# Kernel optimization log

Hardware: AMD Instinct MI355X
Metric: run time of the kernel (lower is better)

Reference implementation:

```python
import jax, jax.numpy as jnp
import numpy as np

WS = 32          # window_size
STRIDE = 16
OUTPUT = 224
GRADE_N = 6

def _dct_mat(size):
    i = np.arange(size)[:, None]
    j = np.arange(size)[None, :]
    scale = np.where(i == 0, np.sqrt(1.0 / size), np.sqrt(2.0 / size))
    return (scale * np.cos((j + 0.5) * np.pi * i / size)).astype(np.float32)

def _gen_filter(start, end, size):
    i = np.arange(size)[:, None]
    j = np.arange(size)[None, :]
    s = i + j
    return np.where((s > end) | (s < start), 0.0, 1.0).astype(np.float32)

# constant (non-learnable) buffers, derived from init hyperparams
_D = jnp.asarray(_dct_mat(WS))                       # [32,32]
_LEVEL_FILT = jnp.asarray(_gen_filter(0, WS * 2, WS))  # level_fliter=[0] -> band (0, 64)
_grade_filts = np.stack([_gen_filter(WS * 2.0 / GRADE_N * i, WS * 2.0 / GRADE_N * (i + 1), WS)
                         for i in range(GRADE_N)])    # [G,32,32]
_ft_num = _grade_filts.sum(axis=(1, 2))               # per-filter normalizer
_weights = (2.0 ** np.arange(GRADE_N)).astype(np.float32)  # w=1, *=2 each pass
_GRADE_FILT_SCALED = jnp.asarray(_grade_filts * (_weights / _ft_num)[:, None, None])  # [G,32,32]

def _unfold(x):
    # x: [B,C,H,W] -> patches [B,L,C,ws,ws], L row-major over (oh, ow), matching torch Unfold
    B, C, H, W = x.shape
    nH = (H - WS) // STRIDE + 1
    nW = (W - WS) // STRIDE + 1
    r = jnp.arange(nH) * STRIDE
    c = jnp.arange(nW) * STRIDE
    rows = r[:, None, None, None] + jnp.arange(WS)[None, None, :, None]  # [nH,1,ws,1]
    cols = c[None, :, None, None] + jnp.arange(WS)[None, None, None, :]  # [1,nW,1,ws]
    p = x[:, :, rows, cols]                       # [B,C,nH,nW,ws,ws]
    p = jnp.transpose(p, (0, 2, 3, 1, 4, 5))      # [B,nH,nW,C,ws,ws]
    return p.reshape(B, nH * nW, C, WS, WS)

def setup_inputs() -> dict:
    key = jax.random.key(0)
    x = jax.random.normal(key, (16, 3, 512, 512), dtype=jnp.float32)
    return {"x": x}

def reference(x):
    B, C, H, W = x.shape
    patches = _unfold(x)                          # [B,L,C,32,32]
    x_dct = _D @ patches @ _D.T                   # batched 32x32 DCT

    # level branch (level_N=1): filter is all-pass band (0,64) but applied faithfully
    level_y = _D.T @ (x_dct * _LEVEL_FILT) @ _D   # [B,L,C,32,32]

    # grading: sum_g w_g/ft_g * sum_{c,i,j} filt_g * log(|dct|+1)
    lx = jnp.log(jnp.abs(x_dct) + 1.0)
    grade = jnp.einsum('blcij,gij->bl', lx, _GRADE_FILT_SCALED)  # [B,L]

    idx = jnp.argsort(grade, axis=-1)             # ascending
    b = jnp.arange(B)
    minmin_i  = idx[:, 0]
    minmin_i1 = idx[:, 1]    # B > 1 branch
    maxmax_i  = idx[:, -1]
    maxmax_i1 = idx[:, -2]   # B > 1 branch

    # gather single patch per image; fold0 with one block == reshape to [B,C,32,32]
    x_minmin  = level_y[b, minmin_i]
    x_maxmax  = level_y[b, maxmax_i]
    x_minmin1 = level_y[b, minmin_i1]
    x_maxmax1 = level_y[b, maxmax_i1]
    return (x_minmin, x_maxmax, x_minmin1, x_maxmax1)
```

## Files before the change

kernel.cpp:

```cpp
#include <hip/hip_runtime.h>
#include <cstdint>

constexpr double kPI  = 3.14159265358979323846264338327950288;
constexpr double kLN2 = 0.69314718055994530941723212145818;
constexpr double cos_poly(double x) {
    double x2 = x * x, term = 1.0, sum = 1.0;
    for (int n = 1; n <= 13; ++n) { term *= -x2 / double((2 * n - 1) * (2 * n)); sum += term; }
    return sum;
}
constexpr double cos_idx(int a) {
    a &= 127;
    if (a <= 32)  return  cos_poly(a * kPI / 64.0);
    if (a <= 64)  return -cos_poly((64 - a) * kPI / 64.0);
    if (a <= 96)  return -cos_poly((a - 64) * kPI / 64.0);
    return cos_poly((128 - a) * kPI / 64.0);
}
constexpr double csqrt(double v) {
    double x = 1.0;
    for (int i = 0; i < 60; ++i) x = 0.5 * (x + v / x);
    return x;
}
constexpr float Dij(int i, int j) {
    double sc = (i == 0) ? csqrt(1.0 / 32.0) : 0.25;
    int a = ((2 * j + 1) * i) & 127;
    return (float)(sc * cos_idx(a));
}
struct OddT { float d[256]; };
constexpr OddT make_odd() { OddT t{}; for (int m = 0; m < 16; ++m) for (int k = 0; k < 16; ++k) t.d[m*16+k] = Dij(2*m+1, k); return t; }
struct E8T { float d[64]; };
constexpr E8T make_e2() { E8T t{}; for (int m = 0; m < 8; ++m) for (int k = 0; k < 8; ++k) t.d[m*8+k] = Dij(4*m+2, k); return t; }
struct E4T { float d[16]; };
constexpr E4T make_ee() { E4T t{}; for (int m = 0; m < 4; ++m) for (int k = 0; k < 4; ++k) t.d[m*4+k] = Dij(8*m,   k); return t; }
constexpr E4T make_eo() { E4T t{}; for (int m = 0; m < 4; ++m) for (int k = 0; k < 4; ++k) t.d[m*4+k] = Dij(8*m+4, k); return t; }
struct FTab { float f[64]; };
constexpr FTab make_F() {
    FTab t{};
    const int lo[6] = {0, 11, 22, 32, 43, 54};
    const int hi[6] = {10, 21, 32, 42, 53, 62};
    const int n [6] = {66, 187, 306, 286, 165, 45};
    for (int s = 0; s < 64; ++s) {
        double acc = 0.0, w = 1.0;
        for (int g = 0; g < 6; ++g) { if (s >= lo[g] && s <= hi[g]) acc += w / double(n[g]); w *= 2.0; }
        t.f[s] = (float)(acc * kLN2);
    }
    return t;
}
__device__ constexpr OddT cOdd = make_odd();
__device__ constexpr E8T  cE2  = make_e2();
__device__ constexpr E4T  cEE  = make_ee();
__device__ constexpr E4T  cEO  = make_eo();
__device__ constexpr FTab cF   = make_F();

#define NP  15376
#define NPC 46128
#define LPB 961
#define SST 34

template <typename EMIT>
__device__ __forceinline__ void dct32(float* __restrict__ v, EMIT&& emit) {
    #pragma unroll
    for (int k = 0; k < 16; ++k) { float a = v[k], b = v[31-k]; v[k] = a + b; v[31-k] = a - b; }
    #pragma unroll
    for (int k = 0; k < 8; ++k)  { float a = v[k], b = v[15-k]; v[k] = a + b; v[15-k] = a - b; }
    #pragma unroll
    for (int k = 0; k < 4; ++k)  { float a = v[k], b = v[7-k];  v[k] = a + b; v[7-k]  = a - b; }
    #pragma unroll
    for (int m = 0; m < 16; m += 2) {
        float a = 0.f, b = 0.f;
        #pragma unroll
        for (int k = 0; k < 16; ++k) {
            a = fmaf(cOdd.d[m*16+k],     v[31-k], a);
            b = fmaf(cOdd.d[(m+1)*16+k], v[31-k], b);
        }
        emit(2*m+1, a); emit(2*m+3, b);
    }
    #pragma unroll
    for (int m = 0; m < 8; m += 2) {
        float a = 0.f, b = 0.f;
        #pragma unroll
        for (int k = 0; k < 8; ++k) {
            a = fmaf(cE2.d[m*8+k],     v[15-k], a);
            b = fmaf(cE2.d[(m+1)*8+k], v[15-k], b);
        }
        emit(4*m+2, a); emit(4*m+6, b);
    }
    {
        float a0=0.f,a1=0.f,a2=0.f,a3=0.f,b0=0.f,b1=0.f,b2=0.f,b3=0.f;
        #pragma unroll
        for (int k = 0; k < 4; ++k) {
            a0 = fmaf(cEE.d[0*4+k], v[k],   a0);
            a1 = fmaf(cEE.d[1*4+k], v[k],   a1);
            a2 = fmaf(cEE.d[2*4+k], v[k],   a2);
            a3 = fmaf(cEE.d[3*4+k], v[k],   a3);
            b0 = fmaf(cEO.d[0*4+k], v[7-k], b0);
            b1 = fmaf(cEO.d[1*4+k], v[7-k], b1);
            b2 = fmaf(cEO.d[2*4+k], v[7-k], b2);
            b3 = fmaf(cEO.d[3*4+k], v[7-k], b3);
        }
        emit(0, a0); emit(8, a1); emit(16, a2); emit(24, a3);
        emit(4, b0); emit(12, b1); emit(20, b2); emit(28, b3);
    }
}

__global__ __launch_bounds__(64, 4) void k_grade(const float* __restrict__ x,
                                                 float* __restrict__ partial) {
    __shared__ __align__(16) float sS[2][32 * SST];
    __shared__ float sF[64];
    const int tid = threadIdx.x, g = tid >> 5, lane = tid & 31;
    sF[tid] = cF.f[tid];

    const int tc   = blockIdx.x * 2 + g;
    const int task = tc / 3, c = tc - task * 3;
    const int b  = task / LPB;
    const int l  = task - b * LPB;
    const int ph = l / 31, pw = l - ph * 31;
    const float4* row = (const float4*)(x + (size_t)(b * 3 + c) * 262144
                                          + (ph * 16 + lane) * 512 + pw * 16);
    float* S = sS[g];

    float p[32];
    #pragma unroll
    for (int q = 0; q < 8; ++q) {
        float4 f = row[q];
        p[4*q] = f.x; p[4*q+1] = f.y; p[4*q+2] = f.z; p[4*q+3] = f.w;
    }
    dct32(p, [&](int j, float acc) { S[j * SST + lane] = acc; });
    __syncthreads();

    float u[32];
    #pragma unroll
    for (int h = 0; h < 16; ++h) {
        float2 uu = *(const float2*)&S[lane * SST + 2 * h];
        u[2*h] = uu.x; u[2*h+1] = uu.y;
    }
    float gsum = 0.0f;
    dct32(u, [&](int i, float z) {
        gsum = fmaf(__log2f(fabsf(z) + 1.0f), sF[i + lane], gsum);
    });
    #pragma unroll
    for (int off = 16; off > 0; off >>= 1) gsum += __shfl_down(gsum, off, 32);
    if (lane == 0) partial[tc] = gsum;
}

__global__ __launch_bounds__(256) void k_selgather(const float* __restrict__ partial,
                                                   const float* __restrict__ x,
                                                   float* __restrict__ out) {
    __shared__ unsigned long long smx1[256], smx2[256], smn1[256], smn2[256];
    __shared__ int ssel[4];
    const int b = blockIdx.x, tid = threadIdx.x;
    unsigned long long mx1 = 0, mx2 = 0, mn1 = ~0ULL, mn2 = ~0ULL;
    for (int l = tid; l < LPB; l += 256) {
        const float* pp = partial + (size_t)(b * LPB + l) * 3;
        float gr = pp[0] + pp[1] + pp[2];
        unsigned int bits = __float_as_uint(gr);
        unsigned long long k = ((unsigned long long)bits << 32) | (unsigned int)l;
        if (k > mx1) { mx2 = mx1; mx1 = k; } else if (k > mx2) { mx2 = k; }
        if (k < mn1) { mn2 = mn1; mn1 = k; } else if (k < mn2) { mn2 = k; }
    }
    smx1[tid] = mx1; smx2[tid] = mx2; smn1[tid] = mn1; smn2[tid] = mn2;
    for (int off = 128; off > 0; off >>= 1) {
        __syncthreads();
        if (tid < off) {
            unsigned long long a1 = smx1[tid], a2 = smx2[tid], b1 = smx1[tid + off], b2 = smx2[tid + off];
            unsigned long long lo = a1 < b1 ? a1 : b1, hi = a1 < b1 ? b1 : a1;
            unsigned long long c2 = a2 > b2 ? a2 : b2;
            smx1[tid] = hi; smx2[tid] = lo > c2 ? lo : c2;
            a1 = smn1[tid]; a2 = smn2[tid]; b1 = smn1[tid + off]; b2 = smn2[tid + off];
            lo = a1 < b1 ? a1 : b1; hi = a1 < b1 ? b1 : a1;
            c2 = a2 < b2 ? a2 : b2;
            smn1[tid] = lo; smn2[tid] = hi < c2 ? hi : c2;
        }
    }
    __syncthreads();
    if (tid == 0) {
        ssel[0] = (int)(smn1[0] & 0xffffffffu);
        ssel[1] = (int)(smx1[0] & 0xffffffffu);
        ssel[2] = (int)(smn2[0] & 0xffffffffu);
        ssel[3] = (int)(smx2[0] & 0xffffffffu);
    }
    __syncthreads();

    #pragma unroll
    for (int it = 0; it < 12; ++it) {
        const int q  = it * 256 + tid;
        const int o  = q / 768;
        const int r2 = q - o * 768;
        const int c  = r2 >> 8;
        const int p  = r2 & 255;
        const int i  = p >> 3, j4 = p & 7;
        const int l  = ssel[o];
        const int r0 = (l / 31) * 16, c0 = (l - (l / 31) * 31) * 16;
        const float4 v = *(const float4*)(x + ((size_t)(b * 3 + c) * 512 + r0 + i) * 512 + c0 + 4 * j4);
        *(float4*)(out + (size_t)o * 49152 + b * 3072 + c * 1024 + i * 32 + 4 * j4) = v;
    }
}

extern "C" void kernel_launch(void* const* d_in, const int* in_sizes, int n_in,
                              void* d_out, int out_size, void* d_ws, size_t ws_size,
                              hipStream_t stream) {
    const float* x = (const float*)d_in[0];
    float* out     = (float*)d_out;
    float* partial = (float*)d_ws;
    k_grade    <<<NPC / 2, 64, 0, stream>>>(x, partial);
    k_selgather<<<16,     256, 0, stream>>>(partial, x, out);
}
```

Baseline: 111.7 us.

## Compute patch DCTs with fp16 MFMA instead of scalar butterfly FMAs

Replaces the per-lane scalar butterfly DCT with two stages of 16x16x32 fp16 MFMA matrix multiplies, one full 64-lane wave per patch-channel. A small init kernel prepares fp16 DCT-matrix fragments in workspace, and the grade weights are indexed to match the MFMA output layout. This cuts the FMA-bound arithmetic, but casting inputs and intermediates to fp16 lowers precision and could change the argsort selection on near-ties. It also adds an extra kernel launch.

After: 106.2 us. 1.05x faster.

```diff
diff --git a/kernel.cpp b/kernel.cpp
--- a/kernel.cpp
+++ b/kernel.cpp
@@ -1,5 +1,8 @@
 #include <hip/hip_runtime.h>
 #include <cstdint>
+
+typedef _Float16 f16x8 __attribute__((ext_vector_type(8)));
+typedef float    f32x4 __attribute__((ext_vector_type(4)));
 
 constexpr double kPI  = 3.14159265358979323846264338327950288;
 constexpr double kLN2 = 0.69314718055994530941723212145818;
@@ -20,18 +23,17 @@
     for (int i = 0; i < 60; ++i) x = 0.5 * (x + v / x);
     return x;
 }
-constexpr float Dij(int i, int j) {
-    double sc = (i == 0) ? csqrt(1.0 / 32.0) : 0.25;
-    int a = ((2 * j + 1) * i) & 127;
-    return (float)(sc * cos_idx(a));
-}
-struct OddT { float d[256]; };
-constexpr OddT make_odd() { OddT t{}; for (int m = 0; m < 16; ++m) for (int k = 0; k < 16; ++k) t.d[m*16+k] = Dij(2*m+1, k); return t; }
-struct E8T { float d[64]; };
-constexpr E8T make_e2() { E8T t{}; for (int m = 0; m < 8; ++m) for (int k = 0; k < 8; ++k) t.d[m*8+k] = Dij(4*m+2, k); return t; }
-struct E4T { float d[16]; };
-constexpr E4T make_ee() { E4T t{}; for (int m = 0; m < 4; ++m) for (int k = 0; k < 4; ++k) t.d[m*4+k] = Dij(8*m,   k); return t; }
-constexpr E4T make_eo() { E4T t{}; for (int m = 0; m < 4; ++m) for (int k = 0; k < 4; ++k) t.d[m*4+k] = Dij(8*m+4, k); return t; }
+struct DTab { float d[1024]; };
+constexpr DTab make_D() {
+    DTab t{};
+    const double s0 = csqrt(1.0 / 32.0);
+    for (int i = 0; i < 32; ++i) {
+        double sc = (i == 0) ? s0 : 0.25;
+        for (int j = 0; j < 32; ++j)
+            t.d[i * 32 + j] = (float)(sc * cos_idx(((2 * j + 1) * i) & 127));
+    }
+    return t;
+}
 struct FTab { float f[64]; };
 constexpr FTab make_F() {
     FTab t{};
@@ -45,100 +47,102 @@
     }
     return t;
 }
-__device__ constexpr OddT cOdd = make_odd();
-__device__ constexpr E8T  cE2  = make_e2();
-__device__ constexpr E4T  cEE  = make_ee();
-__device__ constexpr E4T  cEO  = make_eo();
-__device__ constexpr FTab cF   = make_F();
+__device__ constexpr DTab cD = make_D();
+__device__ constexpr FTab cF = make_F();
 
 #define NP  15376
 #define NPC 46128
 #define LPB 961
-#define SST 34
-
-template <typename EMIT>
-__device__ __forceinline__ void dct32(float* __restrict__ v, EMIT&& emit) {
-    #pragma unroll
-    for (int k = 0; k < 16; ++k) { float a = v[k], b = v[31-k]; v[k] = a + b; v[31-k] = a - b; }
-    #pragma unroll
-    for (int k = 0; k < 8; ++k)  { float a = v[k], b = v[15-k]; v[k] = a + b; v[15-k] = a - b; }
-    #pragma unroll
-    for (int k = 0; k < 4; ++k)  { float a = v[k], b = v[7-k];  v[k] = a + b; v[7-k]  = a - b; }
-    #pragma unroll
-    for (int m = 0; m < 16; m += 2) {
-        float a = 0.f, b = 0.f;
+#define TP  36
+
+__global__ __launch_bounds__(128) void k_init(_Float16* __restrict__ dfrag) {
+    const int t = threadIdx.x;
+    const int tile = t >> 6, lane = t & 63;
+    const int m  = 16 * tile + (lane & 15);
+    const int k0 = ((lane >> 4) & 3) * 8;
+    #pragma unroll
+    for (int j = 0; j < 8; ++j)
+        dfrag[t * 8 + j] = (_Float16)cD.d[m * 32 + k0 + j];
+}
+
+__global__ __launch_bounds__(128, 4) void k_grade(const float* __restrict__ x,
+                                                  const _Float16* __restrict__ dfrag,
+                                                  float* __restrict__ partial) {
+    __shared__ __align__(16) float sT[2][32 * TP];
+    __shared__ float sF[64];
+    const int tid  = threadIdx.x;
+    const int wv   = tid >> 6, lane = tid & 63;
+    const int quad = lane >> 4, n = lane & 15;
+    if (tid < 64) sF[tid] = cF.f[tid];
+
+    const int tc   = blockIdx.x * 2 + wv;
+    const int task = tc / 3, c = tc - task * 3;
+    const int b  = task / LPB, l = task - b * LPB;
+    const int ph = l / 31, pw = l - ph * 31;
+
+    const f16x8* DF = (const f16x8*)dfrag;
+    const f16x8 d0 = DF[lane], d1 = DF[64 + lane];
+
+    const float* pp = x + (size_t)(b * 3 + c) * 262144
+                        + (size_t)(ph * 16 + quad * 8) * 512 + pw * 16 + n;
+    f16x8 p0, p1;
+    #pragma unroll
+    for (int j = 0; j < 8; ++j) {
+        p0[j] = (_Float16)pp[j * 512];
+        p1[j] = (_Float16)pp[j * 512 + 16];
+    }
+
+    const f32x4 z4 = {0.f, 0.f, 0.f, 0.f};
+    f32x4 t00 = __builtin_amdgcn_mfma_f32_16x16x32_f16(d0, p0, z4, 0, 0, 0);
+    f32x4 t01 = __builtin_amdgcn_mfma_f32_16x16x32_f16(d0, p1, z4, 0, 0, 0);
+    f32x4 t10 = __builtin_amdgcn_mfma_f32_16x16x32_f16(d1, p0, z4, 0, 0, 0);
+    f32x4 t11 = __builtin_amdgcn_mfma_f32_16x16x32_f16(d1, p1, z4, 0, 0, 0);
+
+    float* S = sT[wv];
+    #pragma unroll
+    for (int r = 0; r < 4; ++r) {
+        S[(quad * 4 + r) * TP + n]           = t00[r];
+        S[(quad * 4 + r) * TP + 16 + n]      = t01[r];
+        S[(16 + quad * 4 + r) * TP + n]      = t10[r];
+        S[(16 + quad * 4 + r) * TP + 16 + n] = t11[r];
+    }
+    __syncthreads();
+
+    f16x8 a0, a1;
+    {
+        const float* rp = &S[n * TP + quad * 8];
+        const float4 x0 = *(const float4*)(rp);
+        const float4 x1 = *(const float4*)(rp + 4);
+        const float4 x2 = *(const float4*)(rp + 16 * TP);
+        const float4 x3 = *(const float4*)(rp + 16 * TP + 4);
+        a0[0]=(_Float16)x0.x; a0[1]=(_Float16)x0.y; a0[2]=(_Float16)x0.z; a0[3]=(_Float16)x0.w;
+        a0[4]=(_Float16)x1.x; a0[5]=(_Float16)x1.y; a0[6]=(_Float16)x1.z; a0[7]=(_Float16)x1.w;
+        a1[0]=(_Float16)x2.x; a1[1]=(_Float16)x2.y; a1[2]=(_Float16)x2.z; a1[3]=(_Float16)x2.w;
+        a1[4]=(_Float16)x3.x; a1[5]=(_Float16)x3.y; a1[6]=(_Float16)x3.z; a1[7]=(_Float16)x3.w;
+    }
+
+    f32x4 q00 = __builtin_amdgcn_mfma_f32_16x16x32_f16(a0, d0, z4, 0, 0, 0);
+    f32x4 q01 = __builtin_amdgcn_mfma_f32_16x16x32_f16(a0, d1, z4, 0, 0, 0);
+    f32x4 q10 = __builtin_amdgcn_mfma_f32_16x16x32_f16(a1, d0, z4, 0, 0, 0);
+    f32x4 q11 = __builtin_amdgcn_mfma_f32_16x16x32_f16(a1, d1, z4, 0, 0, 0);
+
+    const int sb = quad * 4 + n;
+    float W[12];
+    #pragma unroll
+    for (int t2 = 0; t2 < 3; ++t2)
         #pragma unroll
-        for (int k = 0; k < 16; ++k) {
-            a = fmaf(cOdd.d[m*16+k],     v[31-k], a);
-            b = fmaf(cOdd.d[(m+1)*16+k], v[31-k], b);
-        }
-        emit(2*m+1, a); emit(2*m+3, b);
-    }
-    #pragma unroll
-    for (int m = 0; m < 8; m += 2) {
-        float a = 0.f, b = 0.f;
-        #pragma unroll
-        for (int k = 0; k < 8; ++k) {
-            a = fmaf(cE2.d[m*8+k],     v[15-k], a);
-            b = fmaf(cE2.d[(m+1)*8+k], v[15-k], b);
-        }
-        emit(4*m+2, a); emit(4*m+6, b);
-    }
-    {
-        float a0=0.f,a1=0.f,a2=0.f,a3=0.f,b0=0.f,b1=0.f,b2=0.f,b3=0.f;
-        #pragma unroll
-        for (int k = 0; k < 4; ++k) {
-            a0 = fmaf(cEE.d[0*4+k], v[k],   a0);
-            a1 = fmaf(cEE.d[1*4+k], v[k],   a1);
-            a2 = fmaf(cEE.d[2*4+k], v[k],   a2);
-            a3 = fmaf(cEE.d[3*4+k], v[k],   a3);
-            b0 = fmaf(cEO.d[0*4+k], v[7-k], b0);
-            b1 = fmaf(cEO.d[1*4+k], v[7-k], b1);
-            b2 = fmaf(cEO.d[2*4+k], v[7-k], b2);
-            b3 = fmaf(cEO.d[3*4+k], v[7-k], b3);
-        }
-        emit(0, a0); emit(8, a1); emit(16, a2); emit(24, a3);
-        emit(4, b0); emit(12, b1); emit(20, b2); emit(28, b3);
-    }
-}
-
-__global__ __launch_bounds__(64, 4) void k_grade(const float* __restrict__ x,
-                                                 float* __restrict__ partial) {
-    __shared__ __align__(16) float sS[2][32 * SST];
-    __shared__ float sF[64];
-    const int tid = threadIdx.x, g = tid >> 5, lane = tid & 31;
-    sF[tid] = cF.f[tid];
-
-    const int tc   = blockIdx.x * 2 + g;
-    const int task = tc / 3, c = tc - task * 3;
-    const int b  = task / LPB;
-    const int l  = task - b * LPB;
-    const int ph = l / 31, pw = l - ph * 31;
-    const float4* row = (const float4*)(x + (size_t)(b * 3 + c) * 262144
-                                          + (ph * 16 + lane) * 512 + pw * 16);
-    float* S = sS[g];
-
-    float p[32];
-    #pragma unroll
-    for (int q = 0; q < 8; ++q) {
-        float4 f = row[q];
-        p[4*q] = f.x; p[4*q+1] = f.y; p[4*q+2] = f.z; p[4*q+3] = f.w;
-    }
-    dct32(p, [&](int j, float acc) { S[j * SST + lane] = acc; });
-    __syncthreads();
-
-    float u[32];
-    #pragma unroll
-    for (int h = 0; h < 16; ++h) {
-        float2 uu = *(const float2*)&S[lane * SST + 2 * h];
-        u[2*h] = uu.x; u[2*h+1] = uu.y;
-    }
-    float gsum = 0.0f;
-    dct32(u, [&](int i, float z) {
-        gsum = fmaf(__log2f(fabsf(z) + 1.0f), sF[i + lane], gsum);
-    });
-    #pragma unroll
-    for (int off = 16; off > 0; off >>= 1) gsum += __shfl_down(gsum, off, 32);
+        for (int r = 0; r < 4; ++r) W[t2 * 4 + r] = sF[sb + 16 * t2 + r];
+
+    float gsum = 0.f;
+    #pragma unroll
+    for (int r = 0; r < 4; ++r) {
+        gsum = fmaf(__log2f(fabsf(q00[r]) + 1.f), W[r],     gsum);
+        gsum = fmaf(__log2f(fabsf(q01[r]) + 1.f), W[4 + r], gsum);
+        gsum = fmaf(__log2f(fabsf(q10[r]) + 1.f), W[4 + r], gsum);
+        gsum = fmaf(__log2f(fabsf(q11[r]) + 1.f), W[8 + r], gsum);
+    }
+    #pragma unroll
+    for (int off = 32; off > 0; off >>= 1) gsum += __shfl_down(gsum, off, 64);
     if (lane == 0) partial[tc] = gsum;
 }
 
@@ -201,6 +205,8 @@
     const float* x = (const float*)d_in[0];
     float* out     = (float*)d_out;
     float* partial = (float*)d_ws;
-    k_grade    <<<NPC / 2, 64, 0, stream>>>(x, partial);
-    k_selgather<<<16,     256, 0, stream>>>(partial, x, out);
-}
+    _Float16* dfrag = (_Float16*)((char*)d_ws + 47104 * 4);
+    k_init     <<<1,       128, 0, stream>>>(dfrag);
+    k_grade    <<<NPC / 2, 128, 0, stream>>>(x, dfrag, partial);
+    k_selgather<<<16,      256, 0, stream>>>(partial, x, out);
+}
```
